# Performance work log

Measured on AMD Instinct MI355X. Metric: run time of the kernel, lower is better.

The kernel has to match this reference:

```python
import jax, jax.numpy as jnp
import numpy as np

K = 3
STRIDE = 1
PAD = 1

def conv2d(x, w, b, stride, padding):
    out = jax.lax.conv_general_dilated(x, w, (stride, stride), [(padding, padding), (padding, padding)],
                                       dimension_numbers=('NCHW', 'OIHW', 'NCHW'))
    if b is not None:
        out = out + b[None, :, None, None]
    return out

def deform_conv2d(x, offset, mask, weight, stride, padding):
    # torchvision-style modulated deformable conv (offset_groups=1, groups=1)
    B, C, H, W = x.shape
    C2 = weight.shape[0]
    KK = K * K
    Hout, Wout = offset.shape[2], offset.shape[3]
    off = offset.reshape(B, KK, 2, Hout, Wout)  # (dy, dx) pairs per kernel tap
    ky = jnp.repeat(jnp.arange(K), K)  # kernel row per tap [KK]
    kx = jnp.tile(jnp.arange(K), K)    # kernel col per tap [KK]
    base_y = (jnp.arange(Hout) * stride - padding).astype(jnp.float32)
    base_x = (jnp.arange(Wout) * stride - padding).astype(jnp.float32)
    py = off[:, :, 0] + ky[None, :, None, None] + base_y[None, None, :, None]  # [B,KK,Hout,Wout]
    px = off[:, :, 1] + kx[None, :, None, None] + base_x[None, None, None, :]
    y0f = jnp.floor(py); x0f = jnp.floor(px)
    ly = py - y0f; lx = px - x0f
    y0 = y0f.astype(jnp.int32); x0 = x0f.astype(jnp.int32)
    xf = x.reshape(B, C, H * W)

    def corner(yi, xi, wgt):
        valid = (yi >= 0) & (yi < H) & (xi >= 0) & (xi < W)
        idx = (jnp.clip(yi, 0, H - 1) * W + jnp.clip(xi, 0, W - 1)).reshape(B, -1)  # [B, KK*Hout*Wout]
        v = jax.vmap(lambda xb, ib: xb[:, ib])(xf, idx)  # [B, C, KK*Hout*Wout]
        return v * (wgt * valid).reshape(B, 1, -1)

    val = (corner(y0, x0, (1.0 - ly) * (1.0 - lx))
           + corner(y0, x0 + 1, (1.0 - ly) * lx)
           + corner(y0 + 1, x0, ly * (1.0 - lx))
           + corner(y0 + 1, x0 + 1, ly * lx))
    val = val * mask.reshape(B, 1, -1)  # modulation per (tap, spatial)
    val = val.reshape(B, C, KK, Hout, Wout)
    out = jnp.einsum('bckhw,ock->bohw', val, weight.reshape(C2, C, KK))
    return out

def setup_inputs() -> dict:
    key = jax.random.key(0)
    ks = jax.random.split(key, 6)
    B, C1, C2, H, W = 8, 256, 256, 64, 64
    x = jax.random.normal(ks[0], (B, C1, H, W), jnp.float32)
    offset_w = jax.random.normal(ks[1], (2 * K * K, C1, K, K), jnp.float32) * 0.01
    offset_b = jax.random.normal(ks[2], (2 * K * K,), jnp.float32) * 0.5
    mod_w = jax.random.normal(ks[3], (K * K, C1, K, K), jnp.float32) * 0.01
    mod_b = jnp.zeros((K * K,), jnp.float32)
    reg_w = jax.random.normal(ks[4], (C2, C1, K, K), jnp.float32) * np.float32(1.0 / np.sqrt(C1 * K * K))
    return {"x": x, "offset_w": offset_w, "offset_b": offset_b, "mod_w": mod_w, "mod_b": mod_b, "reg_w": reg_w}

def reference(x, offset_w, offset_b, mod_w, mod_b, reg_w):
    h, w = x.shape[2], x.shape[3]
    max_offset = max(h, w) / 4.0
    offset = jnp.clip(conv2d(x, offset_w, offset_b, STRIDE, PAD), -max_offset, max_offset)
    modulator = jax.nn.sigmoid(conv2d(x, mod_w, mod_b, STRIDE, PAD))
    return deform_conv2d(x, offset, modulator, reg_w, STRIDE, PAD)
```

## Files before the change

### kernel.cpp

```cpp
#include <hip/hip_runtime.h>
#include <math.h>

#define BB 8
#define CIN 256
#define COUT 256
#define HH 64
#define WW 64
#define OCM 27
#define KTOT 2304
#define NKT 72

typedef unsigned int u32;
typedef unsigned short u16;

#define WS_XBF 0
#define WS_W2 16777216
#define WS_W2OM 17956864
#define WS_OFFMOD 18104320

__device__ __forceinline__ u16 f2bf(float f) {
    u32 u = __float_as_uint(f);
    u32 r = (u + 0x7FFFu + ((u >> 16) & 1u)) >> 16;
    return (u16)r;
}

typedef __attribute__((address_space(1))) const unsigned int* gptr_t;
typedef __attribute__((address_space(3))) unsigned int* lptr_t;
__device__ __forceinline__ void gl2lds16(const void* g, void* l) {
    __builtin_amdgcn_global_load_lds((gptr_t)g, (lptr_t)l, 16, 0, 0);
}

typedef __attribute__((ext_vector_type(8))) short frag;
typedef __attribute__((ext_vector_type(4))) float f4;

__device__ __forceinline__ int sw_off(int row, int oct) {
    return (row << 5) + ((oct ^ ((row >> 1) & 3)) << 3);
}

#define BARRIER_RAW() do { asm volatile("" ::: "memory"); \
    __builtin_amdgcn_s_barrier(); asm volatile("" ::: "memory"); } while (0)

__global__ __launch_bounds__(256) void k_nhwc3(const float* __restrict__ x,
                                               u16* __restrict__ xbf) {
    const int y = blockIdx.x, b = blockIdx.y;
    __shared__ float T[64][65];
    const int t = threadIdx.x;
    const int wl = t & 63, g = t >> 6;
    const int pr = wl & 31, wsub = wl >> 5;
    u32* xo = (u32*)xbf;
    for (int c0 = 0; c0 < 256; c0 += 64) {
#pragma unroll
        for (int i = 0; i < 16; ++i) {
            int c = g + i * 4;
            T[c][wl] = x[(((size_t)(b * 256 + c0 + c)) << 12) + (y << 6) + wl];
        }
        __syncthreads();
#pragma unroll
        for (int j = 0; j < 8; ++j) {
            int w = j * 8 + g * 2 + wsub;
            u32 v = (u32)f2bf(T[2 * pr][w]) | ((u32)f2bf(T[2 * pr + 1][w]) << 16);
            xo[((((size_t)b << 12) + (y << 6) + w) << 7) + (c0 >> 1) + pr] = v;
        }
        __syncthreads();
    }
}

__global__ void k_pack_w2(const float* __restrict__ rw, u16* __restrict__ w2) {
    int o = blockIdx.x * blockDim.x + threadIdx.x;
    if (o >= NKT * COUT * 32) return;
    int kk = o & 31;
    int n = (o >> 5) & 255;
    int kt = o >> 13;
    int k = kt * 32 + kk;
    int tap = k >> 8;
    int c = k & 255;
    w2[o] = f2bf(rw[n * KTOT + c * 9 + tap]);
}

__global__ void k_pack_w2om(const float* __restrict__ ow, const float* __restrict__ mw,
                            u16* __restrict__ w2om) {
    int o = blockIdx.x * blockDim.x + threadIdx.x;
    if (o >= NKT * 32 * 32) return;
    int kk = o & 31;
    int oc = (o >> 5) & 31;
    int kt = o >> 10;
    int k = kt * 32 + kk;
    int tap = k >> 8;
    int c = k & 255;
    float v = 0.f;
    if (oc < 18) v = ow[oc * KTOT + c * 9 + tap];
    else if (oc < 27) v = mw[(oc - 18) * KTOT + c * 9 + tap];
    w2om[o] = f2bf(v);
}

__global__ __launch_bounds__(512, 4) void k_offmod6(
    const u16* __restrict__ xbf, const u16* __restrict__ w2om,
    const float* __restrict__ ob, const float* __restrict__ mb,
    float* __restrict__ offmod)
{
    const int b = blockIdx.x & 7, h = blockIdx.x >> 3;
    const int t = threadIdx.x;
    const int lane = t & 63, wv = t >> 6;
    const int hf = wv >> 2;
    const int wl4 = wv & 3;
    const int th = t & 255;
    const int fr = lane & 15, q = lane >> 4;
    const int wm = wl4 << 4;
    const int mg = th >> 2, oct = th & 3;

    __shared__ u16 AsB[2][2][64 * 32];
    __shared__ u16 BsB[2][2][32 * 32];
    __shared__ float red[64][33];

    const u16* xb = xbf + ((size_t)b << 20);
    const int kbase = hf * 36;

    auto loadA = [&](int kt, uint4* r) {
        int tap = kt >> 3;
        int yy = h + tap / 3 - 1, xx = mg + tap % 3 - 1;
        int c0 = ((kt & 7) << 5) + (oct << 3);
        uint4 v = make_uint4(0, 0, 0, 0);
        if ((unsigned)yy < HH && (unsigned)xx < WW)
            v = *(const uint4*)(xb + (((size_t)yy << 6) + xx) * 256 + c0);
        *r = v;
    };
    auto loadB = [&](int kt, uint4* r) {
        if (th < 128) *r = *(const uint4*)(w2om + (size_t)kt * 1024 + (th >> 2) * 32 + (th & 3) * 8);
    };
    auto storeAB = [&](int buf, uint4* rA, uint4* rB) {
        *(uint4*)&AsB[hf][buf][sw_off(mg, oct)] = *rA;
        if (th < 128) *(uint4*)&BsB[hf][buf][sw_off(th >> 2, th & 3)] = *rB;
    };

    f4 acc[2];
    acc[0] = (f4){0.f, 0.f, 0.f, 0.f};
    acc[1] = (f4){0.f, 0.f, 0.f, 0.f};

    uint4 rA0, rB0, rA1, rB1;
    loadA(kbase, &rA0); loadB(kbase, &rB0);
    storeAB(0, &rA0, &rB0);
    loadA(kbase + 1, &rA1); loadB(kbase + 1, &rB1);
    asm volatile("s_waitcnt lgkmcnt(0)" ::: "memory");

    auto body = [&](int i, int p, uint4* cA, uint4* cB, uint4* nA, uint4* nB) {
        BARRIER_RAW();
        frag a  = *(const frag*)&AsB[hf][p][sw_off(wm + fr, q)];
        frag b0 = *(const frag*)&BsB[hf][p][sw_off(fr, q)];
        frag b1 = *(const frag*)&BsB[hf][p][sw_off(16 + fr, q)];
        if (i + 2 < 36) { loadA(kbase + i + 2, nA); loadB(kbase + i + 2, nB); }
        if (i + 1 < 36) storeAB(1 - p, cA, cB);
        acc[0] = __builtin_amdgcn_mfma_f32_16x16x32_bf16(a, b0, acc[0], 0, 0, 0);
        acc[1] = __builtin_amdgcn_mfma_f32_16x16x32_bf16(a, b1, acc[1], 0, 0, 0);
        asm volatile("s_waitcnt lgkmcnt(0)" ::: "memory");
    };
    for (int i = 0; i < 36; i += 2) {
        body(i, 0, &rA1, &rB1, &rA0, &rB0);
        body(i + 1, 1, &rA0, &rB0, &rA1, &rB1);
    }

    if (hf == 1) {
#pragma unroll
        for (int ni = 0; ni < 2; ++ni)
#pragma unroll
            for (int r = 0; r < 4; ++r)
                red[wm + q * 4 + r][ni * 16 + fr] = acc[ni][r];
    }
    __syncthreads();
    if (hf == 0) {
#pragma unroll
        for (int ni = 0; ni < 2; ++ni) {
            int oc = ni * 16 + fr;
            if (oc >= OCM) continue;
            bool is_off = oc < 18;
            float bias = is_off ? ob[oc] : mb[oc - 18];
            float4 v;
            float* vp = (float*)&v;
#pragma unroll
            for (int r = 0; r < 4; ++r) {
                float s = acc[ni][r] + red[wm + q * 4 + r][oc] + bias;
                vp[r] = is_off ? fminf(fmaxf(s, -16.f), 16.f)
                               : 1.f / (1.f + __expf(-s));
            }
            *(float4*)&offmod[(((size_t)b * OCM + oc) << 12) + (h << 6) + wm + q * 4] = v;
        }
    }
}

__global__ __launch_bounds__(512, 4) void k_deform7(
    const u16* __restrict__ xbf, const float* __restrict__ offmod,
    const u16* __restrict__ w2, float* __restrict__ out)
{
    const int t = threadIdx.x;
    const int b = blockIdx.x & 7, h = blockIdx.x >> 3;
    const int lane = t & 63, wv = t >> 6;

    __shared__ int   SIDX[9][4][64];
    __shared__ float SW[9][4][64];
    __shared__ u16 AsB[2][64 * 32];
    __shared__ u16 BsB[2][256 * 32];

    const float* om = offmod + (size_t)b * OCM * 4096;
    for (int e = t; e < 9 * 64; e += 512) {
        int m = e & 63, tap = e >> 6;
        float dy = om[(tap * 2) * 4096 + h * 64 + m];
        float dx = om[(tap * 2 + 1) * 4096 + h * 64 + m];
        float mv = om[(18 + tap) * 4096 + h * 64 + m];
        float py = dy + (float)(tap / 3) + (float)(h - 1);
        float px = dx + (float)(tap % 3) + (float)(m - 1);
        float y0f = floorf(py), x0f = floorf(px);
        float ly = py - y0f, lx = px - x0f;
        int y0 = (int)y0f, x0 = (int)x0f;
        int   ysr[2] = {y0, y0 + 1};
        int   xsr[2] = {x0, x0 + 1};
        float wy[2] = {1.f - ly, ly};
        float wx[2] = {1.f - lx, lx};
#pragma unroll
        for (int r = 0; r < 4; ++r) {
            int yy = ysr[r >> 1], xx = xsr[r & 1];
            bool ok = ((unsigned)yy < HH) && ((unsigned)xx < WW);
            int yc = min(max(yy, 0), HH - 1);
            int xc = min(max(xx, 0), WW - 1);
            SIDX[tap][r][m] = yc * WW + xc;
            SW[tap][r][m] = ok ? (wy[r >> 1] * wx[r & 1] * mv) : 0.f;
        }
    }
    __syncthreads();

    if (wv < 4) {
        const int fr = lane & 15, q = lane >> 4;
        const int wn = wv << 6;

        f4 acc[4][4];
#pragma unroll
        for (int mi = 0; mi < 4; ++mi)
#pragma unroll
            for (int ni = 0; ni < 4; ++ni) acc[mi][ni] = (f4){0.f, 0.f, 0.f, 0.f};

        for (int kt = 0; kt < NKT; ++kt) {
            const int p = kt & 1;
            BARRIER_RAW();
            frag a[4];
#pragma unroll
            for (int mi = 0; mi < 4; ++mi)
                a[mi] = *(const frag*)&AsB[p][sw_off(mi * 16 + fr, q)];
#pragma unroll
            for (int nh = 0; nh < 2; ++nh) {
                frag b0 = *(const frag*)&BsB[p][sw_off(wn + nh * 32 + fr, q)];
                frag b1 = *(const frag*)&BsB[p][sw_off(wn + nh * 32 + 16 + fr, q)];
#pragma unroll
                for (int mi = 0; mi < 4; ++mi) {
                    acc[mi][nh * 2]     = __builtin_amdgcn_mfma_f32_16x16x32_bf16(
                        a[mi], b0, acc[mi][nh * 2], 0, 0, 0);
                    acc[mi][nh * 2 + 1] = __builtin_amdgcn_mfma_f32_16x16x32_bf16(
                        a[mi], b1, acc[mi][nh * 2 + 1], 0, 0, 0);
                }
            }
        }

#pragma unroll
        for (int ni = 0; ni < 4; ++ni) {
            int n_g = wn + ni * 16 + fr;
            float* outn = out + (((size_t)b * COUT + n_g) << 12) + (h << 6);
#pragma unroll
            for (int mi = 0; mi < 4; ++mi) {
                int wl = mi * 16 + q * 4;
                *(float4*)&outn[wl] = make_float4(acc[mi][ni][0], acc[mi][ni][1],
                                                  acc[mi][ni][2], acc[mi][ni][3]);
            }
        }
    } else {
        const int pt = t - 256;
        const int mg = pt >> 2, oct = pt & 3;
        const int pwv = wv - 4;
        const int ko_sw = (lane & 3) ^ ((lane >> 3) & 3);
        const u16* xpl = xbf + ((size_t)b << 20);

        auto stageB = [&](int kt, int buf) {
            const u16* src = w2 + ((size_t)kt << 13);
#pragma unroll
            for (int j = 0; j < 4; ++j) {
                int n = (pwv << 6) + (j << 4) + (lane >> 2);
                u16* dst = &BsB[buf][((pwv << 6) + (j << 4)) << 5];
                gl2lds16(src + n * 32 + ko_sw * 8, dst);
            }
        };
        auto loadCorners = [&](int kt, uint4 (&cr)[4]) {
            int tap = kt >> 3;
            int c0 = ((kt & 7) << 5) + (oct << 3);
            const u16* base = xpl + c0;
#pragma unroll
            for (int r = 0; r < 4; ++r)
                cr[r] = *(const uint4*)(base + ((size_t)SIDX[tap][r][mg] << 8));
        };
        auto interpStore = [&](int kt, int buf, uint4 (&cr)[4]) {
            int tap = kt >> 3;
            float va[8];
#pragma unroll
            for (int j = 0; j < 8; ++j) va[j] = 0.f;
#pragma unroll
            for (int r = 0; r < 4; ++r) {
                float s = SW[tap][r][mg];
                u32 uu[4] = {cr[r].x, cr[r].y, cr[r].z, cr[r].w};
#pragma unroll
                for (int jj = 0; jj < 4; ++jj) {
                    va[2 * jj]     += s * __uint_as_float(uu[jj] << 16);
                    va[2 * jj + 1] += s * __uint_as_float(uu[jj] & 0xFFFF0000u);
                }
            }
            u32 pk[4];
#pragma unroll
            for (int jp = 0; jp < 4; ++jp)
                pk[jp] = (u32)f2bf(va[2 * jp]) | ((u32)f2bf(va[2 * jp + 1]) << 16);
            *(uint4*)&AsB[buf][sw_off(mg, oct)] = make_uint4(pk[0], pk[1], pk[2], pk[3]);
        };

        uint4 cr0[4], cr1[4], cr2[4];
        stageB(0, 0);
        loadCorners(0, cr0);
        loadCorners(1, cr1);
        loadCorners(2, cr2);
        interpStore(0, 0, cr0);
        asm volatile("s_waitcnt lgkmcnt(0)" ::: "memory");

        auto pstep = [&](int kt, int p, uint4 (&cur)[4], uint4 (&nxt)[4]) {
            if (kt + 2 < NKT) asm volatile("s_waitcnt vmcnt(4)" ::: "memory");
            else              asm volatile("s_waitcnt vmcnt(0)" ::: "memory");
            BARRIER_RAW();
            if (kt + 1 < NKT) stageB(kt + 1, 1 - p);
            if (kt + 3 < NKT) loadCorners(kt + 3, nxt);
            if (kt + 1 < NKT) interpStore(kt + 1, 1 - p, cur);
            asm volatile("s_waitcnt lgkmcnt(0)" ::: "memory");
        };
        for (int kt = 0; kt < NKT; kt += 6) {
            pstep(kt,     0, cr1, cr0);
            pstep(kt + 1, 1, cr2, cr1);
            pstep(kt + 2, 0, cr0, cr2);
            pstep(kt + 3, 1, cr1, cr0);
            pstep(kt + 4, 0, cr2, cr1);
            pstep(kt + 5, 1, cr0, cr2);
        }
    }
}

extern "C" void kernel_launch(void* const* d_in, const int* in_sizes, int n_in,
                              void* d_out, int out_size, void* d_ws, size_t ws_size,
                              hipStream_t stream) {
    const float* x  = (const float*)d_in[0];
    const float* ow = (const float*)d_in[1];
    const float* ob = (const float*)d_in[2];
    const float* mw = (const float*)d_in[3];
    const float* mb = (const float*)d_in[4];
    const float* rw = (const float*)d_in[5];
    float* out = (float*)d_out;
    char* ws = (char*)d_ws;

    u16*   xbf    = (u16*)(ws + WS_XBF);
    u16*   w2     = (u16*)(ws + WS_W2);
    u16*   w2om   = (u16*)(ws + WS_W2OM);
    float* offmod = (float*)(ws + WS_OFFMOD);

    k_nhwc3<<<dim3(HH, BB), 256, 0, stream>>>(x, xbf);
    k_pack_w2<<<(NKT * COUT * 32 + 255) / 256, 256, 0, stream>>>(rw, w2);
    k_pack_w2om<<<(NKT * 32 * 32 + 255) / 256, 256, 0, stream>>>(ow, mw, w2om);
    k_offmod6<<<dim3(512), 512, 0, stream>>>(xbf, w2om, ob, mb, offmod);
    k_deform7<<<dim3(512), 512, 0, stream>>>(xbf, offmod, w2, out);
}
```

Before: 183.8 us.

## Switch to fp16 with packed bilinear math and two-row deform tiles

Replaces bf16 with fp16 throughout: x conversion, weight packing and the MFMA intrinsics. Bilinear interpolation now runs on packed half2 multiply-adds instead of fp32 unpacking, and corner indices and weights are packed into one uint4 table entry. The deform kernel now handles two output rows per block with 1024 threads, halving the grid. Each B weight tile is reused across 128 pixels, which reduces weight staging traffic per output. The cost is fp16 range and precision risk, plus a larger block that may lower occupancy.

```diff
diff --git a/kernel.cpp b/kernel.cpp
--- a/kernel.cpp
+++ b/kernel.cpp
@@ -12,16 +12,16 @@
 
 typedef unsigned int u32;
 typedef unsigned short u16;
+typedef _Float16 f16;
 
 #define WS_XBF 0
 #define WS_W2 16777216
 #define WS_W2OM 17956864
 #define WS_OFFMOD 18104320
 
-__device__ __forceinline__ u16 f2bf(float f) {
-    u32 u = __float_as_uint(f);
-    u32 r = (u + 0x7FFFu + ((u >> 16) & 1u)) >> 16;
-    return (u16)r;
+__device__ __forceinline__ u16 f2h(float f) {
+    f16 h = (f16)f;
+    return __builtin_bit_cast(u16, h);
 }
 
 typedef __attribute__((address_space(1))) const unsigned int* gptr_t;
@@ -30,7 +30,8 @@
     __builtin_amdgcn_global_load_lds((gptr_t)g, (lptr_t)l, 16, 0, 0);
 }
 
-typedef __attribute__((ext_vector_type(8))) short frag;
+typedef __attribute__((ext_vector_type(8))) f16 frag;
+typedef __attribute__((ext_vector_type(2))) f16 h2;
 typedef __attribute__((ext_vector_type(4))) float f4;
 
 __device__ __forceinline__ int sw_off(int row, int oct) {
@@ -58,7 +59,7 @@
 #pragma unroll
         for (int j = 0; j < 8; ++j) {
             int w = j * 8 + g * 2 + wsub;
-            u32 v = (u32)f2bf(T[2 * pr][w]) | ((u32)f2bf(T[2 * pr + 1][w]) << 16);
+            u32 v = (u32)f2h(T[2 * pr][w]) | ((u32)f2h(T[2 * pr + 1][w]) << 16);
             xo[((((size_t)b << 12) + (y << 6) + w) << 7) + (c0 >> 1) + pr] = v;
         }
         __syncthreads();
@@ -74,7 +75,7 @@
     int k = kt * 32 + kk;
     int tap = k >> 8;
     int c = k & 255;
-    w2[o] = f2bf(rw[n * KTOT + c * 9 + tap]);
+    w2[o] = f2h(rw[n * KTOT + c * 9 + tap]);
 }
 
 __global__ void k_pack_w2om(const float* __restrict__ ow, const float* __restrict__ mw,
@@ -90,7 +91,7 @@
     float v = 0.f;
     if (oc < 18) v = ow[oc * KTOT + c * 9 + tap];
     else if (oc < 27) v = mw[(oc - 18) * KTOT + c * 9 + tap];
-    w2om[o] = f2bf(v);
+    w2om[o] = f2h(v);
 }
 
 __global__ __launch_bounds__(512, 4) void k_offmod6(
@@ -149,8 +150,8 @@
         frag b1 = *(const frag*)&BsB[hf][p][sw_off(16 + fr, q)];
         if (i + 2 < 36) { loadA(kbase + i + 2, nA); loadB(kbase + i + 2, nB); }
         if (i + 1 < 36) storeAB(1 - p, cA, cB);
-        acc[0] = __builtin_amdgcn_mfma_f32_16x16x32_bf16(a, b0, acc[0], 0, 0, 0);
-        acc[1] = __builtin_amdgcn_mfma_f32_16x16x32_bf16(a, b1, acc[1], 0, 0, 0);
+        acc[0] = __builtin_amdgcn_mfma_f32_16x16x32_f16(a, b0, acc[0], 0, 0, 0);
+        acc[1] = __builtin_amdgcn_mfma_f32_16x16x32_f16(a, b1, acc[1], 0, 0, 0);
         asm volatile("s_waitcnt lgkmcnt(0)" ::: "memory");
     };
     for (int i = 0; i < 36; i += 2) {
@@ -186,27 +187,28 @@
     }
 }
 
-__global__ __launch_bounds__(512, 4) void k_deform7(
+__global__ __launch_bounds__(1024, 4) void k_deform8(
     const u16* __restrict__ xbf, const float* __restrict__ offmod,
     const u16* __restrict__ w2, float* __restrict__ out)
 {
     const int t = threadIdx.x;
-    const int b = blockIdx.x & 7, h = blockIdx.x >> 3;
+    const int b = blockIdx.x & 7, hp = blockIdx.x >> 3;
+    const int h0 = hp << 1;
     const int lane = t & 63, wv = t >> 6;
 
-    __shared__ int   SIDX[9][4][64];
-    __shared__ float SW[9][4][64];
-    __shared__ u16 AsB[2][64 * 32];
+    __shared__ uint4 STAB[9][128];
+    __shared__ u16 AsB[2][128 * 32];
     __shared__ u16 BsB[2][256 * 32];
 
     const float* om = offmod + (size_t)b * OCM * 4096;
-    for (int e = t; e < 9 * 64; e += 512) {
-        int m = e & 63, tap = e >> 6;
-        float dy = om[(tap * 2) * 4096 + h * 64 + m];
-        float dx = om[(tap * 2 + 1) * 4096 + h * 64 + m];
-        float mv = om[(18 + tap) * 4096 + h * 64 + m];
-        float py = dy + (float)(tap / 3) + (float)(h - 1);
-        float px = dx + (float)(tap % 3) + (float)(m - 1);
+    for (int e = t; e < 9 * 128; e += 1024) {
+        int m = e & 127, tap = e >> 7;
+        int hh = h0 + (m >> 6), ww = m & 63;
+        float dy = om[(tap * 2) * 4096 + hh * 64 + ww];
+        float dx = om[(tap * 2 + 1) * 4096 + hh * 64 + ww];
+        float mv = om[(18 + tap) * 4096 + hh * 64 + ww];
+        float py = dy + (float)(tap / 3) + (float)(hh - 1);
+        float px = dx + (float)(tap % 3) + (float)(ww - 1);
         float y0f = floorf(py), x0f = floorf(px);
         float ly = py - y0f, lx = px - x0f;
         int y0 = (int)y0f, x0 = (int)x0f;
@@ -214,104 +216,112 @@
         int   xsr[2] = {x0, x0 + 1};
         float wy[2] = {1.f - ly, ly};
         float wx[2] = {1.f - lx, lx};
+        u16 idx[4]; f16 wgt[4];
 #pragma unroll
         for (int r = 0; r < 4; ++r) {
             int yy = ysr[r >> 1], xx = xsr[r & 1];
             bool ok = ((unsigned)yy < HH) && ((unsigned)xx < WW);
             int yc = min(max(yy, 0), HH - 1);
             int xc = min(max(xx, 0), WW - 1);
-            SIDX[tap][r][m] = yc * WW + xc;
-            SW[tap][r][m] = ok ? (wy[r >> 1] * wx[r & 1] * mv) : 0.f;
-        }
+            idx[r] = (u16)(yc * WW + xc);
+            wgt[r] = (f16)(ok ? (wy[r >> 1] * wx[r & 1] * mv) : 0.f);
+        }
+        uint4 tv;
+        tv.x = (u32)idx[0] | ((u32)idx[1] << 16);
+        tv.y = (u32)idx[2] | ((u32)idx[3] << 16);
+        h2 w01 = {wgt[0], wgt[1]};
+        h2 w23 = {wgt[2], wgt[3]};
+        tv.z = __builtin_bit_cast(u32, w01);
+        tv.w = __builtin_bit_cast(u32, w23);
+        STAB[tap][m] = tv;
     }
     __syncthreads();
 
-    if (wv < 4) {
+    if (wv < 8) {
         const int fr = lane & 15, q = lane >> 4;
-        const int wn = wv << 6;
-
-        f4 acc[4][4];
-#pragma unroll
-        for (int mi = 0; mi < 4; ++mi)
-#pragma unroll
-            for (int ni = 0; ni < 4; ++ni) acc[mi][ni] = (f4){0.f, 0.f, 0.f, 0.f};
+        const int wn = wv << 5;
+
+        f4 acc[8][2];
+#pragma unroll
+        for (int mi = 0; mi < 8; ++mi) {
+            acc[mi][0] = (f4){0.f, 0.f, 0.f, 0.f};
+            acc[mi][1] = (f4){0.f, 0.f, 0.f, 0.f};
+        }
 
         for (int kt = 0; kt < NKT; ++kt) {
             const int p = kt & 1;
             BARRIER_RAW();
-            frag a[4];
-#pragma unroll
-            for (int mi = 0; mi < 4; ++mi)
-                a[mi] = *(const frag*)&AsB[p][sw_off(mi * 16 + fr, q)];
-#pragma unroll
-            for (int nh = 0; nh < 2; ++nh) {
-                frag b0 = *(const frag*)&BsB[p][sw_off(wn + nh * 32 + fr, q)];
-                frag b1 = *(const frag*)&BsB[p][sw_off(wn + nh * 32 + 16 + fr, q)];
-#pragma unroll
-                for (int mi = 0; mi < 4; ++mi) {
-                    acc[mi][nh * 2]     = __builtin_amdgcn_mfma_f32_16x16x32_bf16(
-                        a[mi], b0, acc[mi][nh * 2], 0, 0, 0);
-                    acc[mi][nh * 2 + 1] = __builtin_amdgcn_mfma_f32_16x16x32_bf16(
-                        a[mi], b1, acc[mi][nh * 2 + 1], 0, 0, 0);
-                }
-            }
-        }
-
-#pragma unroll
-        for (int ni = 0; ni < 4; ++ni) {
+            frag b0 = *(const frag*)&BsB[p][sw_off(wn + fr, q)];
+            frag b1 = *(const frag*)&BsB[p][sw_off(wn + 16 + fr, q)];
+#pragma unroll
+            for (int mi = 0; mi < 8; ++mi) {
+                frag a = *(const frag*)&AsB[p][sw_off(mi * 16 + fr, q)];
+                acc[mi][0] = __builtin_amdgcn_mfma_f32_16x16x32_f16(a, b0, acc[mi][0], 0, 0, 0);
+                acc[mi][1] = __builtin_amdgcn_mfma_f32_16x16x32_f16(a, b1, acc[mi][1], 0, 0, 0);
+            }
+        }
+
+#pragma unroll
+        for (int ni = 0; ni < 2; ++ni) {
             int n_g = wn + ni * 16 + fr;
-            float* outn = out + (((size_t)b * COUT + n_g) << 12) + (h << 6);
-#pragma unroll
-            for (int mi = 0; mi < 4; ++mi) {
-                int wl = mi * 16 + q * 4;
-                *(float4*)&outn[wl] = make_float4(acc[mi][ni][0], acc[mi][ni][1],
-                                                  acc[mi][ni][2], acc[mi][ni][3]);
+            float* outn = out + (((size_t)b * COUT + n_g) << 12) + (h0 << 6);
+#pragma unroll
+            for (int mi = 0; mi < 8; ++mi) {
+                int off = ((mi >> 2) << 6) + ((mi & 3) << 4) + (q << 2);
+                *(float4*)&outn[off] = make_float4(acc[mi][ni][0], acc[mi][ni][1],
+                                                   acc[mi][ni][2], acc[mi][ni][3]);
             }
         }
     } else {
-        const int pt = t - 256;
+        const int pt = t - 512;
         const int mg = pt >> 2, oct = pt & 3;
-        const int pwv = wv - 4;
+        const int pwv = wv - 8;
         const int ko_sw = (lane & 3) ^ ((lane >> 3) & 3);
         const u16* xpl = xbf + ((size_t)b << 20);
 
         auto stageB = [&](int kt, int buf) {
             const u16* src = w2 + ((size_t)kt << 13);
 #pragma unroll
-            for (int j = 0; j < 4; ++j) {
-                int n = (pwv << 6) + (j << 4) + (lane >> 2);
-                u16* dst = &BsB[buf][((pwv << 6) + (j << 4)) << 5];
+            for (int j = 0; j < 2; ++j) {
+                int base = (pwv << 5) + (j << 4);
+                int n = base + (lane >> 2);
+                u16* dst = &BsB[buf][base << 5];
                 gl2lds16(src + n * 32 + ko_sw * 8, dst);
             }
         };
         auto loadCorners = [&](int kt, uint4 (&cr)[4]) {
             int tap = kt >> 3;
             int c0 = ((kt & 7) << 5) + (oct << 3);
+            uint2 iv = *(const uint2*)&STAB[tap][mg];
             const u16* base = xpl + c0;
-#pragma unroll
-            for (int r = 0; r < 4; ++r)
-                cr[r] = *(const uint4*)(base + ((size_t)SIDX[tap][r][mg] << 8));
+            cr[0] = *(const uint4*)(base + ((size_t)(iv.x & 0xFFFFu) << 8));
+            cr[1] = *(const uint4*)(base + ((size_t)(iv.x >> 16) << 8));
+            cr[2] = *(const uint4*)(base + ((size_t)(iv.y & 0xFFFFu) << 8));
+            cr[3] = *(const uint4*)(base + ((size_t)(iv.y >> 16) << 8));
         };
         auto interpStore = [&](int kt, int buf, uint4 (&cr)[4]) {
             int tap = kt >> 3;
-            float va[8];
-#pragma unroll
-            for (int j = 0; j < 8; ++j) va[j] = 0.f;
-#pragma unroll
-            for (int r = 0; r < 4; ++r) {
-                float s = SW[tap][r][mg];
-                u32 uu[4] = {cr[r].x, cr[r].y, cr[r].z, cr[r].w};
-#pragma unroll
-                for (int jj = 0; jj < 4; ++jj) {
-                    va[2 * jj]     += s * __uint_as_float(uu[jj] << 16);
-                    va[2 * jj + 1] += s * __uint_as_float(uu[jj] & 0xFFFF0000u);
-                }
-            }
-            u32 pk[4];
-#pragma unroll
-            for (int jp = 0; jp < 4; ++jp)
-                pk[jp] = (u32)f2bf(va[2 * jp]) | ((u32)f2bf(va[2 * jp + 1]) << 16);
-            *(uint4*)&AsB[buf][sw_off(mg, oct)] = make_uint4(pk[0], pk[1], pk[2], pk[3]);
+            uint2 wvp = *(const uint2*)(((const u32*)&STAB[tap][mg]) + 2);
+            h2 w01 = __builtin_bit_cast(h2, wvp.x);
+            h2 w23 = __builtin_bit_cast(h2, wvp.y);
+            h2 s0 = {w01[0], w01[0]};
+            h2 s1 = {w01[1], w01[1]};
+            h2 s2 = {w23[0], w23[0]};
+            h2 s3 = {w23[1], w23[1]};
+            const u32* c0p = (const u32*)&cr[0];
+            const u32* c1p = (const u32*)&cr[1];
+            const u32* c2p = (const u32*)&cr[2];
+            const u32* c3p = (const u32*)&cr[3];
+            u32 o[4];
+#pragma unroll
+            for (int jj = 0; jj < 4; ++jj) {
+                h2 v = s0 * __builtin_bit_cast(h2, c0p[jj]);
+                v += s1 * __builtin_bit_cast(h2, c1p[jj]);
+                v += s2 * __builtin_bit_cast(h2, c2p[jj]);
+                v += s3 * __builtin_bit_cast(h2, c3p[jj]);
+                o[jj] = __builtin_bit_cast(u32, v);
+            }
+            *(uint4*)&AsB[buf][sw_off(mg, oct)] = make_uint4(o[0], o[1], o[2], o[3]);
         };
 
         uint4 cr0[4], cr1[4], cr2[4];
@@ -363,5 +373,5 @@
     k_pack_w2<<<(NKT * COUT * 32 + 255) / 256, 256, 0, stream>>>(rw, w2);
     k_pack_w2om<<<(NKT * 32 * 32 + 255) / 256, 256, 0, stream>>>(ow, mw, w2om);
     k_offmod6<<<dim3(512), 512, 0, stream>>>(xbf, w2om, ob, mb, offmod);
-    k_deform7<<<dim3(512), 512, 0, stream>>>(xbf, offmod, w2, out);
-}
+    k_deform8<<<dim3(256), 1024, 0, stream>>>(xbf, offmod, w2, out);
+}
```

Result: faster. 169.8 us (-7.6%).
